# Performance work log

Measured on AMD Instinct MI355X. Metric: run time of the kernel, lower is better.

The kernel has to match this reference:

```python
import jax, jax.numpy as jnp
import numpy as np

DIM = 768
HEADS = 12
HEAD_DIM = DIM // HEADS
SCALE = HEAD_DIM ** -0.5
ALPHA = 0.1


def setup_inputs() -> dict:
    key = jax.random.key(0)
    ks = jax.random.split(key, 6)
    B, N, C = 16, 577, DIM
    x = jax.random.normal(ks[0], (B, N, C), dtype=jnp.float32)
    attn_weight = jax.random.uniform(ks[1], (B, N - 1), dtype=jnp.float32)
    w_qkv = jax.random.normal(ks[2], (C, 3 * C), dtype=jnp.float32) * (C ** -0.5)
    b_qkv = jnp.zeros((3 * C,), dtype=jnp.float32)
    w_proj = jax.random.normal(ks[3], (C, C), dtype=jnp.float32) * (C ** -0.5)
    b_proj = jnp.zeros((C,), dtype=jnp.float32)
    return {"x": x, "attn_weight": attn_weight, "w_qkv": w_qkv, "b_qkv": b_qkv,
            "w_proj": w_proj, "b_proj": b_proj}


def reference(x, attn_weight, w_qkv, b_qkv, w_proj, b_proj):
    B, N, C = x.shape
    H, D = HEADS, HEAD_DIM
    qkv = (x @ w_qkv + b_qkv).reshape(B, N, 3, H, D)
    qkv = jnp.transpose(qkv, (2, 0, 3, 1, 4))  # [3, B, H, N, D]
    q, k, v = qkv[0], qkv[1], qkv[2]
    attn = jnp.einsum('bhnd,bhmd->bhnm', q, k) * SCALE  # [B,H,N,N]
    patch_attn = attn[:, :, 0, 1:]  # pre-softmax CLS->patch scores
    # reweight CLS row (excluding CLS->CLS) before softmax
    w = attn_weight[:, None, None, :]  # [B,1,1,N-1]
    cls_row = attn[:, :, 0:1, 1:] * (w * ALPHA + (1.0 - ALPHA))
    attn = attn.at[:, :, 0:1, 1:].set(cls_row)
    attn = jax.nn.softmax(attn, axis=-1)
    out = jnp.einsum('bhnm,bhmd->bhnd', attn, v)
    out = jnp.transpose(out, (0, 2, 1, 3)).reshape(B, N, C)
    out = out @ w_proj + b_proj
    return out, patch_attn
```

## Files before the change

### kernel.cpp

```cpp
#include <hip/hip_runtime.h>
#include <hip/hip_bf16.h>
#include <math.h>

#define B_    16
#define N_    577
#define C_    768
#define H_    12
#define D_    64
#define M_    (B_ * N_)
#define MP_   9344
#define QKVN  2304
#define NP_   640
#define SCALE 0.125f
#define ALPHA 0.1f
#define OUT0  (B_ * N_ * C_)

#define NB_CONV 3504
#define NB_T1   1728
#define NB_T2   576

typedef __attribute__((ext_vector_type(8))) short short8;
typedef __attribute__((ext_vector_type(4))) float f32x4;
typedef __hip_bfloat16 bf16;

__device__ __forceinline__ float exp2fast(float x) {
    return __builtin_amdgcn_exp2f(x);
}

__device__ __forceinline__ void load16(const void* g, void* l) {
    __builtin_amdgcn_global_load_lds(
        (const __attribute__((address_space(1))) unsigned int*)g,
        (__attribute__((address_space(3))) unsigned int*)l, 16, 0, 0);
}

__device__ __forceinline__ f32x4 mfma16(short8 a, short8 b, f32x4 c) {
    return __builtin_amdgcn_mfma_f32_16x16x32_bf16(a, b, c, 0, 0, 0);
}

#define FENCE() asm volatile("" ::: "memory")
#define BARRIER() do { FENCE(); __builtin_amdgcn_s_barrier(); FENCE(); } while (0)

__global__ __launch_bounds__(256) void prep(const float* __restrict__ x,
                                            bf16* __restrict__ xb,
                                            const float* __restrict__ wq,
                                            bf16* __restrict__ wqT,
                                            const float* __restrict__ wp,
                                            bf16* __restrict__ wpT) {
    __shared__ float tile[32][33];
    const int bid = blockIdx.x;
    if (bid < NB_CONV) {
        int idx = bid * 256 + threadIdx.x;
        int m = idx / 96;
        bf16 tmp[8];
        if (m < M_) {
            float4 f0 = ((const float4*)x)[idx * 2];
            float4 f1 = ((const float4*)x)[idx * 2 + 1];
            tmp[0] = __float2bfloat16(f0.x);
            tmp[1] = __float2bfloat16(f0.y);
            tmp[2] = __float2bfloat16(f0.z);
            tmp[3] = __float2bfloat16(f0.w);
            tmp[4] = __float2bfloat16(f1.x);
            tmp[5] = __float2bfloat16(f1.y);
            tmp[6] = __float2bfloat16(f1.z);
            tmp[7] = __float2bfloat16(f1.w);
        } else {
            #pragma unroll
            for (int i = 0; i < 8; i++) tmp[i] = __float2bfloat16(0.f);
        }
        *(uint4*)(xb + (size_t)idx * 8) = *(const uint4*)tmp;
        return;
    }
    const float* src; bf16* dst; int C, R, bx, by;
    if (bid < NB_CONV + NB_T1) {
        int r = bid - NB_CONV;
        bx = r % 72; by = r / 72; src = wq; dst = wqT; R = 768; C = QKVN;
    } else {
        int r = bid - NB_CONV - NB_T1;
        bx = r % 24; by = r / 24; src = wp; dst = wpT; R = 768; C = 768;
    }
    int cb = bx * 32, rb = by * 32;
    int tx = threadIdx.x & 31, ty = threadIdx.x >> 5;
    #pragma unroll
    for (int i = 0; i < 32; i += 8)
        tile[ty + i][tx] = src[(size_t)(rb + ty + i) * C + cb + tx];
    __syncthreads();
    #pragma unroll
    for (int i = 0; i < 32; i += 8)
        dst[(size_t)(cb + ty + i) * R + rb + tx] = __float2bfloat16(tile[tx][ty + i]);
}

__global__ __launch_bounds__(256, 4) void gemm128(const bf16* __restrict__ A,
                                                  const bf16* __restrict__ BT,
                                                  const float* __restrict__ bias,
                                                  bf16* __restrict__ q,
                                                  bf16* __restrict__ kk,
                                                  bf16* __restrict__ vt,
                                                  float* __restrict__ out,
                                                  int mode, int nby) {
    __shared__ __align__(16) char smem[35840];

    const int nwg = gridDim.x;
    const int orig = blockIdx.x;
    const int xcd = orig & 7, ii = orig >> 3;
    const int qq = nwg >> 3, rr = nwg & 7;
    const int wg = (xcd < rr ? xcd * (qq + 1) : rr * (qq + 1) + (xcd - rr) * qq) + ii;
    const int mb = wg / nby;
    const int nb = wg - mb * nby;
    const int m0 = mb * 128, n0 = nb * 128;
    const int t = threadIdx.x, lane = t & 63, w = t >> 6;
    const int wr = w >> 1, wc = w & 1;
    const int r16 = lane & 15, quad = lane >> 4;

    f32x4 acc[4][4];
    #pragma unroll
    for (int i = 0; i < 4; i++)
        #pragma unroll
        for (int j = 0; j < 4; j++) acc[i][j] = (f32x4)(0.f);

    const int lrow = lane >> 3;
    const int clog = ((lane & 7) ^ lrow) << 4;
    const char* gA = (const char*)A  + (size_t)(m0 + w * 32 + lrow) * 1536 + clog;
    const char* gB = (const char*)BT + (size_t)(n0 + w * 32 + lrow) * 1536 + clog;

    auto stage = [&](int k2) {
        const int kc = k2 * 128;
        #pragma unroll
        for (int i = 0; i < 4; i++) {
            char* dA = (char*)smem + w * 4096 + i * 1024;
            load16(gA + (size_t)i * 12288 + kc, dA);
            load16(gB + (size_t)i * 12288 + kc, dA + 16384);
        }
    };

    stage(0);
    asm volatile("s_waitcnt vmcnt(0)" ::: "memory");
    BARRIER();

    const int sw = r16 & 7;
    const int g0 = (quad ^ sw) << 4;
    const int g1 = ((quad ^ 4) ^ sw) << 4;

    #pragma unroll 1
    for (int k = 0; k < 12; k++) {
        const char* Ap = (const char*)smem + (wr * 64 + r16) * 128;
        const char* Bp = (const char*)smem + 16384 + (wc * 64 + r16) * 128;

        short8 a[4], b[4];
        #pragma unroll
        for (int mi = 0; mi < 4; mi++) a[mi] = *(const short8*)(Ap + mi * 2048 + g0);
        #pragma unroll
        for (int nj = 0; nj < 4; nj++) b[nj] = *(const short8*)(Bp + nj * 2048 + g0);
        __builtin_amdgcn_s_setprio(1);
        #pragma unroll
        for (int mi = 0; mi < 4; mi++)
            #pragma unroll
            for (int nj = 0; nj < 4; nj++)
                acc[mi][nj] = mfma16(a[mi], b[nj], acc[mi][nj]);
        __builtin_amdgcn_s_setprio(0);

        #pragma unroll
        for (int mi = 0; mi < 4; mi++) a[mi] = *(const short8*)(Ap + mi * 2048 + g1);
        #pragma unroll
        for (int nj = 0; nj < 4; nj++) b[nj] = *(const short8*)(Bp + nj * 2048 + g1);
        __builtin_amdgcn_s_setprio(1);
        #pragma unroll
        for (int mi = 0; mi < 4; mi++)
            #pragma unroll
            for (int nj = 0; nj < 4; nj++)
                acc[mi][nj] = mfma16(a[mi], b[nj], acc[mi][nj]);
        __builtin_amdgcn_s_setprio(0);

        BARRIER();
        if (k < 11) {
            stage(k + 1);
            asm volatile("s_waitcnt vmcnt(0)" ::: "memory");
            BARRIER();
        }
    }

    float bs[4];
    #pragma unroll
    for (int nj = 0; nj < 4; nj++) bs[nj] = bias[n0 + wc * 64 + nj * 16 + r16];

    if (mode == 1) {
        #pragma unroll
        for (int mi = 0; mi < 4; mi++) {
            #pragma unroll
            for (int nj = 0; nj < 4; nj++) {
                #pragma unroll
                for (int r = 0; r < 4; r++) {
                    int m = m0 + wr * 64 + mi * 16 + quad * 4 + r;
                    if (m >= M_) continue;
                    int cc = n0 + wc * 64 + nj * 16 + r16;
                    out[(size_t)m * 768 + cc] = acc[mi][nj][r] + bs[nj];
                }
            }
        }
        return;
    }

    bf16* Tt = (bf16*)smem;
    #pragma unroll
    for (int mi = 0; mi < 4; mi++) {
        #pragma unroll
        for (int nj = 0; nj < 4; nj++) {
            bf16 pk[4];
            #pragma unroll
            for (int r = 0; r < 4; r++)
                pk[r] = __float2bfloat16(acc[mi][nj][r] + bs[nj]);
            int ccl = wc * 64 + nj * 16 + r16;
            int ml4 = wr * 64 + mi * 16 + quad * 4;
            *(uint2*)&Tt[ccl * 140 + ml4] = *(const uint2*)pk;
        }
    }
    __syncthreads();

    const int part = nb / 6;
    if (part < 2) {
        int nl = t & 127, half = t >> 7;
        int m = m0 + nl;
        if (m < M_) {
            int b = m / N_, n = m - b * N_;
            int h = (nb % 6) * 2 + half;
            bf16* dst = (part == 0 ? q : kk) + ((size_t)(b * H_ + h) * N_ + n) * 64;
            #pragma unroll
            for (int d8 = 0; d8 < 8; d8++) {
                bf16 tv[8];
                #pragma unroll
                for (int dd = 0; dd < 8; dd++)
                    tv[dd] = Tt[(half * 64 + d8 * 8 + dd) * 140 + nl];
                *(uint4*)(dst + d8 * 8) = *(const uint4*)tv;
            }
        }
    } else {
        int dr = t >> 1, seg = t & 1;
        int rem = (nb % 6) * 128 + dr;
        int h = rem >> 6, d = rem & 63;
        int mb2 = m0 + seg * 64;
        int b = mb2 / N_;
        int n = mb2 - b * N_;
        const bf16* src = Tt + dr * 140 + seg * 64;
        int i = 0;
        while (i < 64 && mb2 + i < M_) {
            if (n == N_) { b++; n = 0; }
            bf16* drow = vt + ((size_t)(b * H_ + h) * 64 + d) * NP_;
            if ((n & 7) == 0 && n + 8 <= N_ && i + 8 <= 64 && mb2 + i + 8 <= M_) {
                bf16 tv[8];
                #pragma unroll
                for (int dd = 0; dd < 8; dd++) tv[dd] = src[i + dd];
                *(uint4*)(drow + n) = *(const uint4*)tv;
                i += 8; n += 8;
            } else {
                drow[n] = src[i]; i++; n++;
            }
        }
    }
}

__global__ __launch_bounds__(256) void attn_mfma(const bf16* __restrict__ q,
                                                 const bf16* __restrict__ k,
                                                 const bf16* __restrict__ vt,
                                                 const float* __restrict__ aw,
                                                 bf16* __restrict__ ao,
                                                 float* __restrict__ patch) {
    __shared__ bf16 Kb[4096];
    __shared__ bf16 Vb[4096];
    __shared__ bf16 Pb[4][2048];
    const int orig = blockIdx.x;
    const int wg = (orig & 7) * 120 + (orig >> 3);
    const int bh = wg / 5, qt = wg - bh * 5;
    const int b = bh / H_, h = bh - b * H_;
    const int t = threadIdx.x, lane = t & 63, w = t >> 6;
    const int r16 = lane & 15, quad = lane >> 4;
    const float SC2 = SCALE * 1.44269504f;

    const bf16* kbp = k + (size_t)bh * N_ * 64;
    const bf16* vbp = vt + (size_t)bh * 64 * NP_;

    short8 qa0[2], qa1[2];
    #pragma unroll
    for (int mi = 0; mi < 2; mi++) {
        int qrow = qt * 128 + w * 32 + mi * 16 + r16;
        int qrc = (qrow < N_) ? qrow : (N_ - 1);
        const bf16* qp = q + ((size_t)bh * N_ + qrc) * 64 + quad * 8;
        qa0[mi] = *(const short8*)(qp);
        qa1[mi] = *(const short8*)(qp + 32);
    }

    f32x4 Oacc[2][4];
    #pragma unroll
    for (int mi = 0; mi < 2; mi++)
        #pragma unroll
        for (int d0 = 0; d0 < 4; d0++) Oacc[mi][d0] = (f32x4)(0.f);
    float lrow[2][4];
    #pragma unroll
    for (int mi = 0; mi < 2; mi++)
        #pragma unroll
        for (int rr = 0; rr < 4; rr++) lrow[mi][rr] = 0.f;

    const bool clsrow = (qt == 0) && (w == 0) && (quad == 0);

    auto stage = [&](int kt) {
        #pragma unroll
        for (int is = 0; is < 2; is++) {
            int base = is * 256 + w * 64;
            int slot = base + lane;
            int row = slot >> 3, pos = slot & 7;
            int c = pos ^ (row & 7);
            int jg = kt * 64 + row; if (jg > N_ - 1) jg = N_ - 1;
            load16(kbp + (size_t)jg * 64 + c * 8, &Kb[base * 8]);
        }
        #pragma unroll
        for (int is = 0; is < 2; is++) {
            int base = is * 256 + w * 64;
            int slot = base + lane;
            int row = slot >> 3, pos = slot & 7;
            int c = pos ^ (row & 7);
            load16(vbp + (size_t)row * NP_ + kt * 64 + c * 8, &Vb[base * 8]);
        }
    };

    stage(0);
    __syncthreads();

    for (int kt = 0; kt < 10; kt++) {
        f32x4 S[2][4];
        #pragma unroll
        for (int j0 = 0; j0 < 4; j0++) {
            int row = j0 * 16 + r16;
            const bf16* kpl = &Kb[row * 64];
            short8 kf0 = *(const short8*)(kpl + ((quad ^ (row & 7)) << 3));
            short8 kf1 = *(const short8*)(kpl + (((quad ^ 4) ^ (row & 7)) << 3));
            #pragma unroll
            for (int mi = 0; mi < 2; mi++) {
                f32x4 sa = (f32x4)(0.f);
                sa = mfma16(qa0[mi], kf0, sa);
                sa = mfma16(qa1[mi], kf1, sa);
                S[mi][j0] = sa;
            }
        }

        if (kt < 9) {
            #pragma unroll
            for (int mi = 0; mi < 2; mi++) {
                #pragma unroll
                for (int j0 = 0; j0 < 4; j0++) {
                    float wfac = 1.f;
                    if (mi == 0 && clsrow) {
                        int c = kt * 64 + j0 * 16 + r16;
                        if (c >= 1) {
                            patch[(size_t)bh * (N_ - 1) + (c - 1)] = S[0][j0][0] * SCALE;
                            wfac = aw[b * (N_ - 1) + (c - 1)] * ALPHA + (1.f - ALPHA);
                        }
                    }
                    #pragma unroll
                    for (int rr = 0; rr < 4; rr++) {
                        float v = S[mi][j0][rr] * SC2;
                        if (rr == 0) v *= wfac;
                        float p = exp2fast(v);
                        S[mi][j0][rr] = p;
                        lrow[mi][rr] += p;
                    }
                }
            }
        } else {
            #pragma unroll
            for (int mi = 0; mi < 2; mi++) {
                #pragma unroll
                for (int j0 = 0; j0 < 4; j0++) {
                    int c = kt * 64 + j0 * 16 + r16;
                    bool valid = (c < N_);
                    float wfac = 1.f;
                    if (mi == 0 && clsrow && valid) {
                        patch[(size_t)bh * (N_ - 1) + (c - 1)] = S[0][j0][0] * SCALE;
                        wfac = aw[b * (N_ - 1) + (c - 1)] * ALPHA + (1.f - ALPHA);
                    }
                    #pragma unroll
                    for (int rr = 0; rr < 4; rr++) {
                        float v = S[mi][j0][rr] * SC2;
                        if (rr == 0) v *= wfac;
                        float p = valid ? exp2fast(v) : 0.f;
                        S[mi][j0][rr] = p;
                        lrow[mi][rr] += p;
                    }
                }
            }
        }

        bf16* pw = &Pb[w][0];
        #pragma unroll
        for (int mi = 0; mi < 2; mi++) {
            #pragma unroll
            for (int j0 = 0; j0 < 4; j0++) {
                int cg = j0 * 2 + (r16 >> 3);
                #pragma unroll
                for (int rr = 0; rr < 4; rr++) {
                    int rp = mi * 16 + quad * 4 + rr;
                    pw[rp * 64 + ((cg ^ (rp & 7)) << 3) + (r16 & 7)] =
                        __float2bfloat16(S[mi][j0][rr]);
                }
            }
        }
        short8 pa0[2], pa1[2];
        #pragma unroll
        for (int mi = 0; mi < 2; mi++) {
            int rp = mi * 16 + r16;
            const bf16* pr = pw + rp * 64;
            pa0[mi] = *(const short8*)(pr + ((quad ^ (rp & 7)) << 3));
            pa1[mi] = *(const short8*)(pr + (((quad ^ 4) ^ (rp & 7)) << 3));
        }

        #pragma unroll
        for (int d0 = 0; d0 < 4; d0++) {
            int row = d0 * 16 + r16;
            const bf16* vpl = &Vb[row * 64];
            short8 vf0 = *(const short8*)(vpl + ((quad ^ (row & 7)) << 3));
            short8 vf1 = *(const short8*)(vpl + (((quad ^ 4) ^ (row & 7)) << 3));
            #pragma unroll
            for (int mi = 0; mi < 2; mi++) {
                Oacc[mi][d0] = mfma16(pa0[mi], vf0, Oacc[mi][d0]);
                Oacc[mi][d0] = mfma16(pa1[mi], vf1, Oacc[mi][d0]);
            }
        }

        __syncthreads();
        if (kt < 9) {
            stage(kt + 1);
            __syncthreads();
        }
    }

    #pragma unroll
    for (int mi = 0; mi < 2; mi++) {
        #pragma unroll
        for (int rr = 0; rr < 4; rr++) {
            float l = lrow[mi][rr];
            l += __shfl_xor(l, 1);
            l += __shfl_xor(l, 2);
            l += __shfl_xor(l, 4);
            l += __shfl_xor(l, 8);
            int n = qt * 128 + w * 32 + mi * 16 + quad * 4 + rr;
            if (n >= N_) continue;
            float inv = 1.f / l;
            #pragma unroll
            for (int d0 = 0; d0 < 4; d0++) {
                ao[((size_t)(b * N_ + n) * H_ + h) * 64 + d0 * 16 + r16] =
                    __float2bfloat16(Oacc[mi][d0][rr] * inv);
            }
        }
    }
}

extern "C" void kernel_launch(void* const* d_in, const int* in_sizes, int n_in,
                              void* d_out, int out_size, void* d_ws, size_t ws_size,
                              hipStream_t stream) {
    const float* x      = (const float*)d_in[0];
    const float* aw     = (const float*)d_in[1];
    const float* w_qkv  = (const float*)d_in[2];
    const float* b_qkv  = (const float*)d_in[3];
    const float* w_proj = (const float*)d_in[4];
    const float* b_proj = (const float*)d_in[5];
    float* out = (float*)d_out;

    char* ws = (char*)d_ws;
    bf16* xbf    = (bf16*)(ws);
    bf16* wqkvT  = (bf16*)(ws + 14352384);
    bf16* wprojT = (bf16*)(ws + 17891328);
    bf16* qv     = (bf16*)(ws + 19070976);
    bf16* kv     = (bf16*)(ws + 33251328);
    bf16* vt     = (bf16*)(ws + 47431680);
    bf16* ao     = xbf;

    prep<<<NB_CONV + NB_T1 + NB_T2, 256, 0, stream>>>(x, xbf, w_qkv, wqkvT, w_proj, wprojT);

    gemm128<<<73 * 18, 256, 0, stream>>>(
        xbf, wqkvT, b_qkv, qv, kv, vt, nullptr, 0, 18);

    attn_mfma<<<H_ * B_ * 5, 256, 0, stream>>>(qv, kv, vt, aw, ao, out + OUT0);

    gemm128<<<73 * 6, 256, 0, stream>>>(
        ao, wprojT, b_proj, nullptr, nullptr, nullptr, out, 1, 6);
}
```

Baseline: 205.9 us.

## Widen QKV GEMM tile to 128x256 so each block reuses A across two column tiles

Adds a dedicated QKV GEMM kernel that computes a 128x256 output tile per block, with two 128x128 accumulator sets sharing the same A fragments. Each A tile is loaded once per two column tiles, which halves A-side global and LDS traffic and halves the block count. The scatter epilogue runs twice through shared memory. The larger LDS footprint (48KB) and doubled accumulators lower occupancy to 3 blocks per CU and leave fewer blocks for load balance. The projection GEMM is reduced to a plain fp32-output kernel.

```diff
diff --git a/kernel.cpp b/kernel.cpp
--- a/kernel.cpp
+++ b/kernel.cpp
@@ -89,14 +89,188 @@
         dst[(size_t)(cb + ty + i) * R + rb + tx] = __float2bfloat16(tile[tx][ty + i]);
 }
 
+__global__ __launch_bounds__(256, 3) void gemm128x2(const bf16* __restrict__ A,
+                                                    const bf16* __restrict__ BT,
+                                                    const float* __restrict__ bias,
+                                                    bf16* __restrict__ q,
+                                                    bf16* __restrict__ kk,
+                                                    bf16* __restrict__ vt,
+                                                    int nby) {
+    __shared__ __align__(16) char smem[49152];
+
+    const int nwg = gridDim.x;
+    const int orig = blockIdx.x;
+    const int xcd = orig & 7, ii = orig >> 3;
+    const int qq = nwg >> 3, rr = nwg & 7;
+    const int wg = (xcd < rr ? xcd * (qq + 1) : rr * (qq + 1) + (xcd - rr) * qq) + ii;
+    const int mb = wg / nby;
+    const int np = wg - mb * nby;
+    const int m0 = mb * 128, n0 = np * 256;
+    const int t = threadIdx.x, lane = t & 63, w = t >> 6;
+    const int wr = w >> 1, wc = w & 1;
+    const int r16 = lane & 15, quad = lane >> 4;
+
+    f32x4 acc[2][4][4];
+    #pragma unroll
+    for (int nt = 0; nt < 2; nt++)
+        #pragma unroll
+        for (int i = 0; i < 4; i++)
+            #pragma unroll
+            for (int j = 0; j < 4; j++) acc[nt][i][j] = (f32x4)(0.f);
+
+    const int lrow = lane >> 3;
+    const int clog = ((lane & 7) ^ lrow) << 4;
+    const char* gA  = (const char*)A  + (size_t)(m0 + w * 32 + lrow) * 1536 + clog;
+    const char* gB0 = (const char*)BT + (size_t)(n0 + w * 32 + lrow) * 1536 + clog;
+    const char* gB1 = gB0 + (size_t)128 * 1536;
+
+    auto stage = [&](int k2) {
+        const int kc = k2 * 128;
+        #pragma unroll
+        for (int i = 0; i < 4; i++) {
+            char* dA = (char*)smem + w * 4096 + i * 1024;
+            load16(gA  + (size_t)i * 12288 + kc, dA);
+            load16(gB0 + (size_t)i * 12288 + kc, dA + 16384);
+            load16(gB1 + (size_t)i * 12288 + kc, dA + 32768);
+        }
+    };
+
+    stage(0);
+    asm volatile("s_waitcnt vmcnt(0)" ::: "memory");
+    BARRIER();
+
+    const int sw = r16 & 7;
+    const int g0 = (quad ^ sw) << 4;
+    const int g1 = ((quad ^ 4) ^ sw) << 4;
+
+    #pragma unroll 1
+    for (int k = 0; k < 12; k++) {
+        const char* Ap = (const char*)smem + (wr * 64 + r16) * 128;
+        const char* Bp = (const char*)smem + 16384 + (wc * 64 + r16) * 128;
+
+        short8 a[4], b[4];
+        #pragma unroll
+        for (int mi = 0; mi < 4; mi++) a[mi] = *(const short8*)(Ap + mi * 2048 + g0);
+        #pragma unroll
+        for (int nj = 0; nj < 4; nj++) b[nj] = *(const short8*)(Bp + nj * 2048 + g0);
+        __builtin_amdgcn_s_setprio(1);
+        #pragma unroll
+        for (int mi = 0; mi < 4; mi++)
+            #pragma unroll
+            for (int nj = 0; nj < 4; nj++)
+                acc[0][mi][nj] = mfma16(a[mi], b[nj], acc[0][mi][nj]);
+        __builtin_amdgcn_s_setprio(0);
+        #pragma unroll
+        for (int nj = 0; nj < 4; nj++) b[nj] = *(const short8*)(Bp + 16384 + nj * 2048 + g0);
+        __builtin_amdgcn_s_setprio(1);
+        #pragma unroll
+        for (int mi = 0; mi < 4; mi++)
+            #pragma unroll
+            for (int nj = 0; nj < 4; nj++)
+                acc[1][mi][nj] = mfma16(a[mi], b[nj], acc[1][mi][nj]);
+        __builtin_amdgcn_s_setprio(0);
+
+        #pragma unroll
+        for (int mi = 0; mi < 4; mi++) a[mi] = *(const short8*)(Ap + mi * 2048 + g1);
+        #pragma unroll
+        for (int nj = 0; nj < 4; nj++) b[nj] = *(const short8*)(Bp + nj * 2048 + g1);
+        __builtin_amdgcn_s_setprio(1);
+        #pragma unroll
+        for (int mi = 0; mi < 4; mi++)
+            #pragma unroll
+            for (int nj = 0; nj < 4; nj++)
+                acc[0][mi][nj] = mfma16(a[mi], b[nj], acc[0][mi][nj]);
+        __builtin_amdgcn_s_setprio(0);
+        #pragma unroll
+        for (int nj = 0; nj < 4; nj++) b[nj] = *(const short8*)(Bp + 16384 + nj * 2048 + g1);
+        __builtin_amdgcn_s_setprio(1);
+        #pragma unroll
+        for (int mi = 0; mi < 4; mi++)
+            #pragma unroll
+            for (int nj = 0; nj < 4; nj++)
+                acc[1][mi][nj] = mfma16(a[mi], b[nj], acc[1][mi][nj]);
+        __builtin_amdgcn_s_setprio(0);
+
+        BARRIER();
+        if (k < 11) {
+            stage(k + 1);
+            asm volatile("s_waitcnt vmcnt(0)" ::: "memory");
+            BARRIER();
+        }
+    }
+
+    bf16* Tt = (bf16*)smem;
+    #pragma unroll 1
+    for (int nt = 0; nt < 2; nt++) {
+        const int cb = np * 2 + nt;
+        float bs[4];
+        #pragma unroll
+        for (int nj = 0; nj < 4; nj++)
+            bs[nj] = bias[cb * 128 + wc * 64 + nj * 16 + r16];
+        __syncthreads();
+        #pragma unroll
+        for (int mi = 0; mi < 4; mi++) {
+            #pragma unroll
+            for (int nj = 0; nj < 4; nj++) {
+                bf16 pk[4];
+                #pragma unroll
+                for (int r = 0; r < 4; r++)
+                    pk[r] = __float2bfloat16(acc[nt][mi][nj][r] + bs[nj]);
+                int ccl = wc * 64 + nj * 16 + r16;
+                int ml4 = wr * 64 + mi * 16 + quad * 4;
+                *(uint2*)&Tt[ccl * 140 + ml4] = *(const uint2*)pk;
+            }
+        }
+        __syncthreads();
+
+        const int part = cb / 6;
+        if (part < 2) {
+            int nl = t & 127, half = t >> 7;
+            int m = m0 + nl;
+            if (m < M_) {
+                int b = m / N_, n = m - b * N_;
+                int h = (cb % 6) * 2 + half;
+                bf16* dst = (part == 0 ? q : kk) + ((size_t)(b * H_ + h) * N_ + n) * 64;
+                #pragma unroll
+                for (int d8 = 0; d8 < 8; d8++) {
+                    bf16 tv[8];
+                    #pragma unroll
+                    for (int dd = 0; dd < 8; dd++)
+                        tv[dd] = Tt[(half * 64 + d8 * 8 + dd) * 140 + nl];
+                    *(uint4*)(dst + d8 * 8) = *(const uint4*)tv;
+                }
+            }
+        } else {
+            int dr = t >> 1, seg = t & 1;
+            int rem = (cb % 6) * 128 + dr;
+            int h = rem >> 6, d = rem & 63;
+            int mb2 = m0 + seg * 64;
+            int b = mb2 / N_;
+            int n = mb2 - b * N_;
+            const bf16* src = Tt + dr * 140 + seg * 64;
+            int i = 0;
+            while (i < 64 && mb2 + i < M_) {
+                if (n == N_) { b++; n = 0; }
+                bf16* drow = vt + ((size_t)(b * H_ + h) * 64 + d) * NP_;
+                if ((n & 7) == 0 && n + 8 <= N_ && i + 8 <= 64 && mb2 + i + 8 <= M_) {
+                    bf16 tv[8];
+                    #pragma unroll
+                    for (int dd = 0; dd < 8; dd++) tv[dd] = src[i + dd];
+                    *(uint4*)(drow + n) = *(const uint4*)tv;
+                    i += 8; n += 8;
+                } else {
+                    drow[n] = src[i]; i++; n++;
+                }
+            }
+        }
+    }
+}
+
 __global__ __launch_bounds__(256, 4) void gemm128(const bf16* __restrict__ A,
                                                   const bf16* __restrict__ BT,
                                                   const float* __restrict__ bias,
-                                                  bf16* __restrict__ q,
-                                                  bf16* __restrict__ kk,
-                                                  bf16* __restrict__ vt,
                                                   float* __restrict__ out,
-                                                  int mode, int nby) {
+                                                  int nby) {
     __shared__ __align__(16) char smem[35840];
 
     const int nwg = gridDim.x;
@@ -182,76 +356,16 @@
     #pragma unroll
     for (int nj = 0; nj < 4; nj++) bs[nj] = bias[n0 + wc * 64 + nj * 16 + r16];
 
-    if (mode == 1) {
-        #pragma unroll
-        for (int mi = 0; mi < 4; mi++) {
-            #pragma unroll
-            for (int nj = 0; nj < 4; nj++) {
-                #pragma unroll
-                for (int r = 0; r < 4; r++) {
-                    int m = m0 + wr * 64 + mi * 16 + quad * 4 + r;
-                    if (m >= M_) continue;
-                    int cc = n0 + wc * 64 + nj * 16 + r16;
-                    out[(size_t)m * 768 + cc] = acc[mi][nj][r] + bs[nj];
-                }
-            }
-        }
-        return;
-    }
-
-    bf16* Tt = (bf16*)smem;
     #pragma unroll
     for (int mi = 0; mi < 4; mi++) {
         #pragma unroll
         for (int nj = 0; nj < 4; nj++) {
-            bf16 pk[4];
-            #pragma unroll
-            for (int r = 0; r < 4; r++)
-                pk[r] = __float2bfloat16(acc[mi][nj][r] + bs[nj]);
-            int ccl = wc * 64 + nj * 16 + r16;
-            int ml4 = wr * 64 + mi * 16 + quad * 4;
-            *(uint2*)&Tt[ccl * 140 + ml4] = *(const uint2*)pk;
-        }
-    }
-    __syncthreads();
-
-    const int part = nb / 6;
-    if (part < 2) {
-        int nl = t & 127, half = t >> 7;
-        int m = m0 + nl;
-        if (m < M_) {
-            int b = m / N_, n = m - b * N_;
-            int h = (nb % 6) * 2 + half;
-            bf16* dst = (part == 0 ? q : kk) + ((size_t)(b * H_ + h) * N_ + n) * 64;
-            #pragma unroll
-            for (int d8 = 0; d8 < 8; d8++) {
-                bf16 tv[8];
-                #pragma unroll
-                for (int dd = 0; dd < 8; dd++)
-                    tv[dd] = Tt[(half * 64 + d8 * 8 + dd) * 140 + nl];
-                *(uint4*)(dst + d8 * 8) = *(const uint4*)tv;
-            }
-        }
-    } else {
-        int dr = t >> 1, seg = t & 1;
-        int rem = (nb % 6) * 128 + dr;
-        int h = rem >> 6, d = rem & 63;
-        int mb2 = m0 + seg * 64;
-        int b = mb2 / N_;
-        int n = mb2 - b * N_;
-        const bf16* src = Tt + dr * 140 + seg * 64;
-        int i = 0;
-        while (i < 64 && mb2 + i < M_) {
-            if (n == N_) { b++; n = 0; }
-            bf16* drow = vt + ((size_t)(b * H_ + h) * 64 + d) * NP_;
-            if ((n & 7) == 0 && n + 8 <= N_ && i + 8 <= 64 && mb2 + i + 8 <= M_) {
-                bf16 tv[8];
-                #pragma unroll
-                for (int dd = 0; dd < 8; dd++) tv[dd] = src[i + dd];
-                *(uint4*)(drow + n) = *(const uint4*)tv;
-                i += 8; n += 8;
-            } else {
-                drow[n] = src[i]; i++; n++;
+            #pragma unroll
+            for (int r = 0; r < 4; r++) {
+                int m = m0 + wr * 64 + mi * 16 + quad * 4 + r;
+                if (m >= M_) continue;
+                int cc = n0 + wc * 64 + nj * 16 + r16;
+                out[(size_t)m * 768 + cc] = acc[mi][nj][r] + bs[nj];
             }
         }
     }
@@ -473,11 +587,11 @@
 
     prep<<<NB_CONV + NB_T1 + NB_T2, 256, 0, stream>>>(x, xbf, w_qkv, wqkvT, w_proj, wprojT);
 
-    gemm128<<<73 * 18, 256, 0, stream>>>(
-        xbf, wqkvT, b_qkv, qv, kv, vt, nullptr, 0, 18);
+    gemm128x2<<<73 * 9, 256, 0, stream>>>(
+        xbf, wqkvT, b_qkv, qv, kv, vt, 9);
 
     attn_mfma<<<H_ * B_ * 5, 256, 0, stream>>>(qv, kv, vt, aw, ao, out + OUT0);
 
     gemm128<<<73 * 6, 256, 0, stream>>>(
-        ao, wprojT, b_proj, nullptr, nullptr, nullptr, out, 1, 6);
-}
+        ao, wprojT, b_proj, out, 6);
+}
```

After: 245.1 us. 1.19x slower.
